# Performance work log

Hardware: AMD Instinct MI355X
Metric: run time of the kernel (lower is better)

The kernel has to match this reference:

```python
import jax, jax.numpy as jnp
import numpy as np

B, T, D, S, H, O = 256, 64, 16, 64, 128, 8

# Tsit5 Butcher tableau (explicit, FSAL; 5th-order solution weights = last stage row)
C_NODES = [0.0, 0.161, 0.327, 0.9, 0.9800255409045097, 1.0, 1.0]
A_TAB = [
    [],
    [0.161],
    [-0.008480655492356989, 0.335480655492357],
    [2.8971530571054935, -6.359448489975075, 4.3622954328695815],
    [5.325864828439257, -11.748883564062828, 7.4955393428898365, -0.09249506636175525],
    [5.86145544294642, -12.92096931784711, 8.159367898576159, -0.071584973281401, -0.028269050394068383],
    [0.09646076681806523, 0.01, 0.4798896504144996, 1.379008574103742, -3.290069515436081, 2.324710524099774],
]
B_SOL = [0.09646076681806523, 0.01, 0.4798896504144996, 1.379008574103742, -3.290069515436081, 2.324710524099774, 0.0]


def setup_inputs() -> dict:
    key = jax.random.key(0)
    ks = jax.random.split(key, 10)
    ts = jnp.linspace(0.0, 1.0, T)
    coeff_d = 0.05 * jax.random.normal(ks[0], (B, T - 1, D), jnp.float32)
    coeff_c = 0.05 * jax.random.normal(ks[1], (B, T - 1, D), jnp.float32)
    coeff_b = 0.2 * jax.random.normal(ks[2], (B, T - 1, D), jnp.float32)
    coeff_a = jax.random.normal(ks[3], (B, T - 1, D), jnp.float32)

    def lin(k, fo, fi):
        s = 1.0 / np.sqrt(fi)
        kw, kb = jax.random.split(k)
        return (jax.random.uniform(kw, (fo, fi), jnp.float32, -s, s),
                jax.random.uniform(kb, (fo,), jnp.float32, -s, s))

    Wi1, bi1 = lin(ks[4], H, D)
    Wi2, bi2 = lin(ks[5], S, H)
    Wf1, bf1 = lin(ks[6], H, S)
    Wf2, bf2 = lin(ks[7], H, H)
    Wf3, bf3 = lin(ks[8], S * D, H)
    Wr, br = lin(ks[9], O, S)
    return dict(ts=ts, coeff_d=coeff_d, coeff_c=coeff_c, coeff_b=coeff_b, coeff_a=coeff_a,
                Wi1=Wi1, bi1=bi1, Wi2=Wi2, bi2=bi2,
                Wf1=Wf1, bf1=bf1, Wf2=Wf2, bf2=bf2, Wf3=Wf3, bf3=bf3, Wr=Wr, br=br)


def _forward(ts, coeff_d, coeff_c, coeff_b, coeff_a,
             Wi1, bi1, Wi2, bi2, Wf1, bf1, Wf2, bf2, Wf3, bf3, Wr, br):
    def vf(y, dxdt):
        # y: (B,S); f(y): (B,S,D) from the MLP (softplus hidden, tanh final); return f(y) @ dx/dt
        h1 = jax.nn.softplus(y @ Wf1.T + bf1)
        h2 = jax.nn.softplus(h1 @ Wf2.T + bf2)
        M = jnp.tanh(h2 @ Wf3.T + bf3).reshape(y.shape[0], S, D)
        return jnp.einsum('bsd,bd->bs', M, dxdt)

    # y0 = initial_mlp(control.evaluate(ts[0])); cubic eval at interval start is coeff_a[:,0]
    x0 = coeff_a[:, 0, :]
    y0 = jax.nn.softplus(x0 @ Wi1.T + bi1) @ Wi2.T + bi2  # (B,S)

    hs = jnp.diff(ts)  # (T-1,)

    def step(y, inp):
        h, cd, cc, cb = inp  # h scalar step size; cd/cc/cb: (B,D) cubic coeffs of this interval
        ks = []
        for j in range(7):
            yj = y
            for m, a in enumerate(A_TAB[j]):
                yj = yj + (h * a) * ks[m]
            frac = C_NODES[j] * h
            dxdt = cb + frac * (2.0 * cc + 3.0 * frac * cd)  # d/dt of cubic interpolation
            ks.append(vf(yj, dxdt))
        y_new = y + h * sum(w * k for w, k in zip(B_SOL, ks))
        return y_new, y_new

    xs = (hs, jnp.swapaxes(coeff_d, 0, 1), jnp.swapaxes(coeff_c, 0, 1), jnp.swapaxes(coeff_b, 0, 1))
    _, ys = jax.lax.scan(step, y0, xs)
    ys = jnp.concatenate([y0[None], ys], axis=0)  # (T,B,S), saved at every ts
    out = ys @ Wr.T + br  # linear readout, identity activation
    return jnp.swapaxes(out, 0, 1)  # (B,T,O)


def reference(ts, coeff_d, coeff_c, coeff_b, coeff_a, Wi1, bi1, Wi2, bi2,
              Wf1, bf1, Wf2, bf2, Wf3, bf3, Wr, br):
    return _forward(ts, coeff_d, coeff_c, coeff_b, coeff_a,
                    Wi1, bi1, Wi2, bi2, Wf1, bf1, Wf2, bf2, Wf3, bf3, Wr, br)
```

## Files before the change

kernel.cpp:

```cpp
#include <hip/hip_runtime.h>
#include <math.h>

typedef _Float16 half_t;
typedef _Float16 half2_t __attribute__((ext_vector_type(2)));
typedef _Float16 half8_t __attribute__((ext_vector_type(8)));
typedef float float4_t __attribute__((ext_vector_type(4)));
typedef int int4v __attribute__((ext_vector_type(4)));

#define T_ 64
#define B_ 256
#define D_ 16
#define S_ 64
#define SP_ 68
#define H_ 128
#define O_ 8
#define NSTEP 63
#define NT 512

#define W3I_OFF 0
#define SWF_OFF 131072
#define W1_OFF  135168
#define W2_OFF  151552

#define H2B 8.0f

#define MFMA16(a, b, c) __builtin_amdgcn_mfma_f32_16x16x32_f16(a, b, c, 0, 0, 0)
#define MFMAI8(a, b, c) __builtin_amdgcn_mfma_i32_16x16x64_i8(a, b, c, 0, 0, 0)

#define BAR_LDS() do { \
  asm volatile("s_waitcnt lgkmcnt(0)" ::: "memory"); \
  __builtin_amdgcn_s_barrier(); \
  asm volatile("" ::: "memory"); \
} while (0)

#if __has_builtin(__builtin_amdgcn_mov_dpp)
#define DPP_ADD(x, ctrl) \
  ((x) + __int_as_float(__builtin_amdgcn_mov_dpp(__float_as_int(x), (ctrl), 0xF, 0xF, true)))
#else
#define DPP_ADD(x, ctrl) ((x) + __shfl_xor((x), (ctrl) == 0xB1 ? 1 : (ctrl) == 0x4E ? 2 : (ctrl) == 0x141 ? 4 : 8))
#endif

__device__ constexpr float AE[6][6] = {
  {0.161f, 0.f, 0.f, 0.f, 0.f, 0.f},
  {-0.008480655492356989f, 0.335480655492357f, 0.f, 0.f, 0.f, 0.f},
  {2.8971530571054935f, -6.359448489975075f, 4.3622954328695815f, 0.f, 0.f, 0.f},
  {5.325864828439257f, -11.748883564062828f, 7.4955393428898365f, -0.09249506636175525f, 0.f, 0.f},
  {5.86145544294642f, -12.92096931784711f, 8.159367898576159f, -0.071584973281401f, -0.028269050394068383f, 0.f},
  {0.09646076681806523f, 0.01f, 0.4798896504144996f, 1.379008574103742f, -3.290069515436081f, 2.324710524099774f}
};
__device__ constexpr float CCn[6] = {0.f, 0.161f, 0.327f, 0.9f, 0.9800255409045097f, 1.f};

__device__ __forceinline__ float softplus_f(float x) {
  return fmaxf(x, 0.f) + __logf(1.f + __expf(-fabsf(x)));
}
__device__ __forceinline__ float tanh_f(float x) {
  float xc = fminf(fmaxf(x, -12.f), 12.f);
  float e = __expf(2.f * xc);
  return (e - 1.f) * __builtin_amdgcn_rcpf(e + 1.f);
}

__global__ __launch_bounds__(256) void convert12_kernel(
    const float* __restrict__ Wf1, const float* __restrict__ Wf2,
    unsigned char* __restrict__ wsb)
{
  half_t* w1h = (half_t*)(wsb + W1_OFF);
  half_t* w2h = (half_t*)(wsb + W2_OFF);
  int q = blockIdx.x * 256 + threadIdx.x;
  if (q < 8192) w1h[q] = (half_t)Wf1[q];
  else if (q < 24576) w2h[q - 8192] = (half_t)Wf2[q - 8192];
}

__global__ __launch_bounds__(256) void convert3_kernel(
    const float* __restrict__ Wf3, unsigned char* __restrict__ wsb)
{
  signed char* w3i = (signed char*)(wsb + W3I_OFF);
  float* swf = (float*)(wsb + SWF_OFF);
  const int tid = threadIdx.x;
  const int wid = tid >> 6;
  const int lane = tid & 63;
  const int row = blockIdx.x * 4 + wid;
  const float a0 = Wf3[row * H_ + 2 * lane];
  const float a1 = Wf3[row * H_ + 2 * lane + 1];
  float m = fmaxf(fabsf(a0), fabsf(a1));
  #pragma unroll
  for (int s = 1; s < 64; s <<= 1) m = fmaxf(m, __shfl_xor(m, s));
  const float sw = fmaxf(m, 1e-20f) * (1.0f / 127.0f);
  const float inv = 1.0f / sw;
  w3i[row * H_ + 2 * lane]     = (signed char)(int)floorf(a0 * inv + 0.5f);
  w3i[row * H_ + 2 * lane + 1] = (signed char)(int)floorf(a1 * inv + 0.5f);
  if (lane == 0) swf[row] = sw;
}

__global__ void __launch_bounds__(NT) __attribute__((amdgpu_waves_per_eu(2, 2)))
cde_kernel_i8(
    const float* __restrict__ ts,
    const float* __restrict__ coeff_d,
    const float* __restrict__ coeff_c,
    const float* __restrict__ coeff_b,
    const float* __restrict__ coeff_a,
    const float* __restrict__ Wi1, const float* __restrict__ bi1,
    const float* __restrict__ Wi2, const float* __restrict__ bi2,
    const float* __restrict__ bf1, const float* __restrict__ bf2,
    const float* __restrict__ bf3,
    const float* __restrict__ Wr, const float* __restrict__ br,
    const unsigned char* __restrict__ wsb,
    float* __restrict__ out)
{
  __shared__ __align__(16) half_t syj_h[S_];
  __shared__ __align__(16) half_t sh1h[H_];
  __shared__ __align__(16) unsigned char sh2b[H_];
  __shared__ __align__(16) float shist[T_][SP_];
  __shared__ float sWr[O_ * S_];
  __shared__ float sbr[O_];
  __shared__ float sx0[D_];
  __shared__ float sini[H_];
  __shared__ float shs[T_];

  const int tid = threadIdx.x;
  const int b = blockIdx.x;
  const int w = tid >> 6;
  const int lane = tid & 63;
  const int q = lane >> 4;
  const int c = lane & 15;

  const signed char* __restrict__ w3i = (const signed char*)(wsb + W3I_OFF);
  const float* __restrict__ swf = (const float*)(wsb + SWF_OFF);
  const half_t* __restrict__ w1p = (const half_t*)(wsb + W1_OFF);
  const half_t* __restrict__ w2p = (const half_t*)(wsb + W2_OFF);

  const int n1 = 16 * w + c;
  half8_t bW1[2], bW2[4];
  int4v bW3i[8][2];
  #pragma unroll
  for (int ks = 0; ks < 2; ++ks)
    bW1[ks] = *(const half8_t*)(w1p + n1 * S_ + ks * 32 + q * 8);
  #pragma unroll
  for (int ks = 0; ks < 4; ++ks)
    bW2[ks] = *(const half8_t*)(w2p + n1 * H_ + ks * 32 + q * 8);
  #pragma unroll
  for (int t = 0; t < 8; ++t) {
    const int r = 16 * (8 * w + t) + c;
    #pragma unroll
    for (int ks = 0; ks < 2; ++ks)
      bW3i[t][ks] = *(const int4v*)(w3i + (size_t)r * H_ + ks * 64 + q * 16);
  }
  const float bf1r = bf1[n1];
  const float bf2r = bf2[n1];
  const int s0 = 8 * w + 2 * q;
  const float bf3r0 = bf3[16 * s0 + c];
  const float bf3r1 = bf3[16 * (s0 + 1) + c];
  const float sw0s = swf[16 * s0 + c] * (H2B / 127.0f);
  const float sw1s = swf[16 * (s0 + 1) + c] * (H2B / 127.0f);

  if (tid < O_ * S_) sWr[tid] = Wr[tid];
  if (tid < O_) sbr[tid] = br[tid];
  if (tid < D_) sx0[tid] = coeff_a[(size_t)b * NSTEP * D_ + tid];
  if (tid < NSTEP) shs[tid] = ts[tid + 1] - ts[tid];
  __syncthreads();
  if (tid < H_) {
    float acc = bi1[tid];
    #pragma unroll
    for (int d = 0; d < D_; ++d) acc += sx0[d] * Wi1[tid * D_ + d];
    sini[tid] = softplus_f(acc);
  }
  __syncthreads();
  if (tid < S_) {
    float acc = bi2[tid];
    for (int h = 0; h < H_; ++h) acc += sini[h] * Wi2[tid * H_ + h];
    shist[0][tid] = acc;
  }
  __syncthreads();

  float yr0 = shist[0][s0];
  float yr1 = shist[0][s0 + 1];
  float kr0[6] = {0.f,0.f,0.f,0.f,0.f,0.f};
  float kr1[6] = {0.f,0.f,0.f,0.f,0.f,0.f};
  if (c == 0) {
    half2_t p; p[0] = (half_t)yr0; p[1] = (half_t)yr1;
    *(half2_t*)(syj_h + s0) = p;
  }
  __syncthreads();

  const float4_t Zv = {0.f, 0.f, 0.f, 0.f};
  const int4v Zi = {0, 0, 0, 0};

  const size_t cbase = (size_t)b * NSTEP * D_ + c;
  float cbv = coeff_b[cbase];
  float ccv = coeff_c[cbase];
  float cdv = coeff_d[cbase];

  for (int t = 0; t < NSTEP; ++t) {
    const int tn = (t + 1 < NSTEP) ? (t + 1) : t;
    const size_t cidxn = cbase + (size_t)tn * D_;
    const float cbn = coeff_b[cidxn];
    const float ccn = coeff_c[cidxn];
    const float cdn = coeff_d[cidxn];

    const float hstep = shs[t];
    float dxj[6];
    #pragma unroll
    for (int j = 0; j < 6; ++j) {
      const float frac = CCn[j] * hstep;
      dxj[j] = cbv + frac * (2.f * ccv + 3.f * frac * cdv);
    }

    #pragma unroll
    for (int j = 0; j < 6; ++j) {
      {
        const half8_t* ap = (const half8_t*)syj_h;
        half8_t a0 = ap[q];
        half8_t a1 = ap[4 + q];
        float4_t acc0 = MFMA16(a0, bW1[0], Zv);
        float4_t acc1 = MFMA16(a1, bW1[1], Zv);
        if (q == 0) sh1h[n1] = (half_t)softplus_f(acc0[0] + acc1[0] + bf1r);
      }
      BAR_LDS();

      {
        const half8_t* ap = (const half8_t*)sh1h;
        half8_t a0 = ap[q], a1 = ap[4 + q], a2 = ap[8 + q], a3 = ap[12 + q];
        float4_t accA = MFMA16(a0, bW2[0], Zv);
        float4_t accB = MFMA16(a1, bW2[1], Zv);
        accA = MFMA16(a2, bW2[2], accA);
        accB = MFMA16(a3, bW2[3], accB);
        if (q == 0) {
          const float h2v = softplus_f(accA[0] + accB[0] + bf2r);
          const int qi = (int)(fminf(h2v, H2B) * (127.0f / H2B) + 0.5f);
          sh2b[n1] = (unsigned char)qi;
        }
      }
      BAR_LDS();

      {
        const int4v a0i = *(const int4v*)(sh2b + 16 * q);
        const int4v a1i = *(const int4v*)(sh2b + 64 + 16 * q);
        int4v iacc[8];
        #pragma unroll
        for (int tt = 0; tt < 8; ++tt) iacc[tt] = MFMAI8(a0i, bW3i[tt][0], Zi);
        #pragma unroll
        for (int tt = 0; tt < 8; ++tt) iacc[tt] = MFMAI8(a1i, bW3i[tt][1], iacc[tt]);

        int i0, i1;
        if (q == 0)      { i0 = iacc[0][0]; i1 = iacc[1][0]; }
        else if (q == 1) { i0 = iacc[2][0]; i1 = iacc[3][0]; }
        else if (q == 2) { i0 = iacc[4][0]; i1 = iacc[5][0]; }
        else             { i0 = iacc[6][0]; i1 = iacc[7][0]; }
        const float v0 = (float)i0 * sw0s;
        const float v1 = (float)i1 * sw1s;

        const float dx = dxj[j];
        float p0 = tanh_f(v0 + bf3r0) * dx;
        float p1 = tanh_f(v1 + bf3r1) * dx;
        p0 = DPP_ADD(p0, 0xB1);   p1 = DPP_ADD(p1, 0xB1);
        p0 = DPP_ADD(p0, 0x4E);   p1 = DPP_ADD(p1, 0x4E);
        p0 = DPP_ADD(p0, 0x141);  p1 = DPP_ADD(p1, 0x141);
        p0 = DPP_ADD(p0, 0x140);  p1 = DPP_ADD(p1, 0x140);

        kr0[j] = p0;
        kr1[j] = p1;
        float sa0 = AE[j][0] * kr0[0];
        float sa1 = AE[j][0] * kr1[0];
        #pragma unroll
        for (int m = 1; m < 6; ++m) if (m <= j) { sa0 = fmaf(AE[j][m], kr0[m], sa0); sa1 = fmaf(AE[j][m], kr1[m], sa1); }
        float yn0 = fmaf(hstep, sa0, yr0);
        float yn1 = fmaf(hstep, sa1, yr1);
        if (j == 5) { yr0 = yn0; yr1 = yn1; }
        if (c == 0) {
          half2_t p; p[0] = (half_t)yn0; p[1] = (half_t)yn1;
          *(half2_t*)(syj_h + s0) = p;
          if (j == 5) {
            float2 f; f.x = yn0; f.y = yn1;
            *(float2*)(&shist[t + 1][s0]) = f;
          }
        }
      }
      BAR_LDS();
    }

    cbv = cbn; ccv = ccn; cdv = cdn;
  }

  __syncthreads();
  {
    const int tt = tid >> 3;
    const int oo = tid & 7;
    const float4* yp = (const float4*)(&shist[tt][0]);
    const float4* wp = (const float4*)(sWr + oo * S_);
    float a0 = 0.f, a1 = 0.f;
    #pragma unroll
    for (int i = 0; i < 16; i += 2) {
      float4 y0 = yp[i], w0 = wp[i];
      float4 y1 = yp[i + 1], w1 = wp[i + 1];
      a0 += y0.x * w0.x + y0.y * w0.y + y0.z * w0.z + y0.w * w0.w;
      a1 += y1.x * w1.x + y1.y * w1.y + y1.z * w1.z + y1.w * w1.w;
    }
    out[((size_t)b * T_ + tt) * O_ + oo] = a0 + a1 + sbr[oo];
  }
}

extern "C" void kernel_launch(void* const* d_in, const int* in_sizes, int n_in,
                              void* d_out, int out_size, void* d_ws, size_t ws_size,
                              hipStream_t stream) {
  const float* ts  = (const float*)d_in[0];
  const float* cd  = (const float*)d_in[1];
  const float* cc  = (const float*)d_in[2];
  const float* cb  = (const float*)d_in[3];
  const float* ca  = (const float*)d_in[4];
  const float* Wi1 = (const float*)d_in[5];
  const float* bi1 = (const float*)d_in[6];
  const float* Wi2 = (const float*)d_in[7];
  const float* bi2 = (const float*)d_in[8];
  const float* Wf1 = (const float*)d_in[9];
  const float* bf1 = (const float*)d_in[10];
  const float* Wf2 = (const float*)d_in[11];
  const float* bf2 = (const float*)d_in[12];
  const float* Wf3 = (const float*)d_in[13];
  const float* bf3 = (const float*)d_in[14];
  const float* Wr  = (const float*)d_in[15];
  const float* br  = (const float*)d_in[16];

  unsigned char* wsb = (unsigned char*)d_ws;
  hipLaunchKernelGGL(convert12_kernel, dim3(96), dim3(256), 0, stream, Wf1, Wf2, wsb);
  hipLaunchKernelGGL(convert3_kernel, dim3(256), dim3(256), 0, stream, Wf3, wsb);
  hipLaunchKernelGGL(cde_kernel_i8, dim3(B_), dim3(NT), 0, stream,
                     ts, cd, cc, cb, ca, Wi1, bi1, Wi2, bi2,
                     bf1, bf2, bf3, Wr, br, wsb, (float*)d_out);
}
```

Before: 423.2 us.

## Split third-layer work across 16 waves per block instead of 8

Doubles the block to 1024 threads so each wave handles 4 of the 64 state rows in the int8 Wf3 MFMA stage instead of 8, halving per-wave MFMA and tanh work on the critical path. The first two layers run only on the first 8 waves, and the others idle at the barriers. This shortens each wave's serial chain in the last stage but adds barrier cost across twice as many waves and lowers occupancy headroom (waves_per_eu set to 4).

```diff
diff --git a/kernel.cpp b/kernel.cpp
--- a/kernel.cpp
+++ b/kernel.cpp
@@ -15,7 +15,7 @@
 #define H_ 128
 #define O_ 8
 #define NSTEP 63
-#define NT 512
+#define NT 1024
 
 #define W3I_OFF 0
 #define SWF_OFF 131072
@@ -91,8 +91,8 @@
   if (lane == 0) swf[row] = sw;
 }
 
-__global__ void __launch_bounds__(NT) __attribute__((amdgpu_waves_per_eu(2, 2)))
-cde_kernel_i8(
+__global__ void __launch_bounds__(NT) __attribute__((amdgpu_waves_per_eu(4, 4)))
+cde_kernel_i8w16(
     const float* __restrict__ ts,
     const float* __restrict__ coeff_d,
     const float* __restrict__ coeff_c,
@@ -128,9 +128,10 @@
   const half_t* __restrict__ w1p = (const half_t*)(wsb + W1_OFF);
   const half_t* __restrict__ w2p = (const half_t*)(wsb + W2_OFF);
 
-  const int n1 = 16 * w + c;
+  const int wh = w & 7;
+  const int n1 = 16 * wh + c;
   half8_t bW1[2], bW2[4];
-  int4v bW3i[8][2];
+  int4v bW3i[4][2];
   #pragma unroll
   for (int ks = 0; ks < 2; ++ks)
     bW1[ks] = *(const half8_t*)(w1p + n1 * S_ + ks * 32 + q * 8);
@@ -138,19 +139,17 @@
   for (int ks = 0; ks < 4; ++ks)
     bW2[ks] = *(const half8_t*)(w2p + n1 * H_ + ks * 32 + q * 8);
   #pragma unroll
-  for (int t = 0; t < 8; ++t) {
-    const int r = 16 * (8 * w + t) + c;
+  for (int t = 0; t < 4; ++t) {
+    const int r = 16 * (4 * w + t) + c;
     #pragma unroll
     for (int ks = 0; ks < 2; ++ks)
       bW3i[t][ks] = *(const int4v*)(w3i + (size_t)r * H_ + ks * 64 + q * 16);
   }
   const float bf1r = bf1[n1];
   const float bf2r = bf2[n1];
-  const int s0 = 8 * w + 2 * q;
+  const int s0 = 4 * w + q;
   const float bf3r0 = bf3[16 * s0 + c];
-  const float bf3r1 = bf3[16 * (s0 + 1) + c];
   const float sw0s = swf[16 * s0 + c] * (H2B / 127.0f);
-  const float sw1s = swf[16 * (s0 + 1) + c] * (H2B / 127.0f);
 
   if (tid < O_ * S_) sWr[tid] = Wr[tid];
   if (tid < O_) sbr[tid] = br[tid];
@@ -172,13 +171,8 @@
   __syncthreads();
 
   float yr0 = shist[0][s0];
-  float yr1 = shist[0][s0 + 1];
   float kr0[6] = {0.f,0.f,0.f,0.f,0.f,0.f};
-  float kr1[6] = {0.f,0.f,0.f,0.f,0.f,0.f};
-  if (c == 0) {
-    half2_t p; p[0] = (half_t)yr0; p[1] = (half_t)yr1;
-    *(half2_t*)(syj_h + s0) = p;
-  }
+  if (c == 0) syj_h[s0] = (half_t)yr0;
   __syncthreads();
 
   const float4_t Zv = {0.f, 0.f, 0.f, 0.f};
@@ -206,7 +200,7 @@
 
     #pragma unroll
     for (int j = 0; j < 6; ++j) {
-      {
+      if (w < 8) {
         const half8_t* ap = (const half8_t*)syj_h;
         half8_t a0 = ap[q];
         half8_t a1 = ap[4 + q];
@@ -216,7 +210,7 @@
       }
       BAR_LDS();
 
-      {
+      if (w < 8) {
         const half8_t* ap = (const half8_t*)sh1h;
         half8_t a0 = ap[q], a1 = ap[4 + q], a2 = ap[8 + q], a3 = ap[12 + q];
         float4_t accA = MFMA16(a0, bW2[0], Zv);
@@ -234,44 +228,35 @@
       {
         const int4v a0i = *(const int4v*)(sh2b + 16 * q);
         const int4v a1i = *(const int4v*)(sh2b + 64 + 16 * q);
-        int4v iacc[8];
+        int4v iacc[4];
         #pragma unroll
-        for (int tt = 0; tt < 8; ++tt) iacc[tt] = MFMAI8(a0i, bW3i[tt][0], Zi);
+        for (int tt = 0; tt < 4; ++tt) iacc[tt] = MFMAI8(a0i, bW3i[tt][0], Zi);
         #pragma unroll
-        for (int tt = 0; tt < 8; ++tt) iacc[tt] = MFMAI8(a1i, bW3i[tt][1], iacc[tt]);
-
-        int i0, i1;
-        if (q == 0)      { i0 = iacc[0][0]; i1 = iacc[1][0]; }
-        else if (q == 1) { i0 = iacc[2][0]; i1 = iacc[3][0]; }
-        else if (q == 2) { i0 = iacc[4][0]; i1 = iacc[5][0]; }
-        else             { i0 = iacc[6][0]; i1 = iacc[7][0]; }
+        for (int tt = 0; tt < 4; ++tt) iacc[tt] = MFMAI8(a1i, bW3i[tt][1], iacc[tt]);
+
+        int i0;
+        if (q == 0)      i0 = iacc[0][0];
+        else if (q == 1) i0 = iacc[1][0];
+        else if (q == 2) i0 = iacc[2][0];
+        else             i0 = iacc[3][0];
         const float v0 = (float)i0 * sw0s;
-        const float v1 = (float)i1 * sw1s;
 
         const float dx = dxj[j];
         float p0 = tanh_f(v0 + bf3r0) * dx;
-        float p1 = tanh_f(v1 + bf3r1) * dx;
-        p0 = DPP_ADD(p0, 0xB1);   p1 = DPP_ADD(p1, 0xB1);
-        p0 = DPP_ADD(p0, 0x4E);   p1 = DPP_ADD(p1, 0x4E);
-        p0 = DPP_ADD(p0, 0x141);  p1 = DPP_ADD(p1, 0x141);
-        p0 = DPP_ADD(p0, 0x140);  p1 = DPP_ADD(p1, 0x140);
+        p0 = DPP_ADD(p0, 0xB1);
+        p0 = DPP_ADD(p0, 0x4E);
+        p0 = DPP_ADD(p0, 0x141);
+        p0 = DPP_ADD(p0, 0x140);
 
         kr0[j] = p0;
-        kr1[j] = p1;
         float sa0 = AE[j][0] * kr0[0];
-        float sa1 = AE[j][0] * kr1[0];
         #pragma unroll
-        for (int m = 1; m < 6; ++m) if (m <= j) { sa0 = fmaf(AE[j][m], kr0[m], sa0); sa1 = fmaf(AE[j][m], kr1[m], sa1); }
+        for (int m = 1; m < 6; ++m) if (m <= j) sa0 = fmaf(AE[j][m], kr0[m], sa0);
         float yn0 = fmaf(hstep, sa0, yr0);
-        float yn1 = fmaf(hstep, sa1, yr1);
-        if (j == 5) { yr0 = yn0; yr1 = yn1; }
+        if (j == 5) yr0 = yn0;
         if (c == 0) {
-          half2_t p; p[0] = (half_t)yn0; p[1] = (half_t)yn1;
-          *(half2_t*)(syj_h + s0) = p;
-          if (j == 5) {
-            float2 f; f.x = yn0; f.y = yn1;
-            *(float2*)(&shist[t + 1][s0]) = f;
-          }
+          syj_h[s0] = (half_t)yn0;
+          if (j == 5) shist[t + 1][s0] = yn0;
         }
       }
       BAR_LDS();
@@ -281,7 +266,7 @@
   }
 
   __syncthreads();
-  {
+  if (tid < 512) {
     const int tt = tid >> 3;
     const int oo = tid & 7;
     const float4* yp = (const float4*)(&shist[tt][0]);
@@ -322,7 +307,7 @@
   unsigned char* wsb = (unsigned char*)d_ws;
   hipLaunchKernelGGL(convert12_kernel, dim3(96), dim3(256), 0, stream, Wf1, Wf2, wsb);
   hipLaunchKernelGGL(convert3_kernel, dim3(256), dim3(256), 0, stream, Wf3, wsb);
-  hipLaunchKernelGGL(cde_kernel_i8, dim3(B_), dim3(NT), 0, stream,
+  hipLaunchKernelGGL(cde_kernel_i8w16, dim3(B_), dim3(NT), 0, stream,
                      ts, cd, cc, cb, ca, Wi1, bi1, Wi2, bi2,
                      bf1, bf2, bf3, Wr, br, wsb, (float*)d_out);
 }
```

New measurement: 434.7 us. +2.7%, slower.
